# Kernel optimization log

Hardware: AMD Instinct MI355X
Metric: run time of the kernel (lower is better)

The kernel has to match this reference:

```python
import jax, jax.numpy as jnp
import numpy as np

B, T, D_MODEL = 2, 192, 512
N_HEADS, D_HEAD = 8, 64
IGNORE = -1000000.0


def setup_inputs() -> dict:
    key = jax.random.key(0)
    ks = jax.random.split(key, 5)
    s = 0.02
    return {
        "x": jax.random.normal(ks[0], (B, T, D_MODEL), dtype=jnp.float32),
        "Wkkq": jax.random.normal(ks[1], (D_MODEL, 3 * N_HEADS * D_HEAD), dtype=jnp.float32) * s,
        "bkkq": jnp.zeros((3 * N_HEADS * D_HEAD,), jnp.float32),
        "Wv1": jax.random.normal(ks[2], (D_MODEL, N_HEADS * D_HEAD), dtype=jnp.float32) * s,
        "bv1": jnp.zeros((N_HEADS * D_HEAD,), jnp.float32),
        "Wv2": jax.random.normal(ks[3], (D_MODEL, N_HEADS * D_HEAD), dtype=jnp.float32) * s,
        "bv2": jnp.zeros((N_HEADS * D_HEAD,), jnp.float32),
        "Wout": jax.random.normal(ks[4], (N_HEADS * D_HEAD, D_MODEL), dtype=jnp.float32) * s,
        "bout": jnp.zeros((D_MODEL,), jnp.float32),
    }


def reference(x, Wkkq, bkkq, Wv1, bv1, Wv2, bv2, Wout, bout):
    b, ts, _ = x.shape
    kkq = x @ Wkkq + bkkq                          # [b, t, 3*n*h]
    k1, k2, q = jnp.split(kkq, 3, axis=-1)
    rs = lambda a: a.reshape(b, ts, N_HEADS, D_HEAD)  # b p n h
    k1, k2, q = rs(k1), rs(k2), rs(q)

    v1 = (x @ Wv1 + bv1).reshape(b, ts, N_HEADS, D_HEAD)
    v2 = (x @ Wv2 + bv2).reshape(b, ts, N_HEADS, D_HEAD)

    # third-order scores: [b, n, s, t, q]
    score_qk = jnp.einsum('btnh,bqnh->bntq', k2, q)   # [b, n, t, q]
    score_kk = jnp.einsum('bsnh,btnh->bnst', k1, k2)  # [b, n, s, t]
    score = score_qk[:, :, None, :, :] + score_kk[..., None]  # [b,n,s,t,q]

    idx = jnp.arange(ts)
    # causal mask: (t > q) | (s > q)  over axes (s, t, q)
    mask = (idx[:, None, None] > idx[None, None, :]) | (idx[None, :, None] > idx[None, None, :])
    score = jnp.where(mask[None, None], IGNORE, score)

    # b n s t q -> b n q (s t), scale by d_head, softmax over flattened (s,t)
    score = jnp.transpose(score, (0, 1, 4, 2, 3)).reshape(b, N_HEADS, ts, ts * ts)
    attn = jax.nn.softmax(score / D_HEAD, axis=-1)

    # v[b, p, t, n, h] = silu(v1)[b,p,n,h] * v2[b,t,n,h]
    v = jax.nn.silu(v1)[:, :, None] * v2[:, None]     # [b, p, t, n, h]
    v = jnp.transpose(v, (0, 3, 4, 1, 2)).reshape(b, N_HEADS, D_HEAD, ts * ts)

    z = jnp.einsum('bnql,bnhl->bqnh', attn, v)        # [b, q, n, h]
    out = z.reshape(b, ts, N_HEADS * D_HEAD) @ Wout + bout
    return out
```

## Files before the change

kernel.cpp:

```cpp
#include <hip/hip_runtime.h>
#include <hip/hip_bf16.h>


constexpr int Tn = 192;
constexpr int DM = 512;
constexpr int NH = 8;
constexpr int HD = 64;
constexpr int TT = Tn * Tn;
constexpr int NC = 8;
constexpr int CS = 24;

typedef __bf16 bf16_t;
typedef bf16_t bf16x8 __attribute__((ext_vector_type(8)));
typedef bf16_t bf16x4 __attribute__((ext_vector_type(4)));
typedef float  f32x4  __attribute__((ext_vector_type(4)));

struct bf16pair { bf16_t h, l; };
__device__ __forceinline__ bf16pair split_bf16(float v) {
    bf16pair r;
    r.h = (bf16_t)v;
    r.l = (bf16_t)(v - (float)r.h);
    return r;
}

__global__ __launch_bounds__(256) void k_convert(
    const float* __restrict__ x,    const float* __restrict__ Wkkq,
    const float* __restrict__ Wv1,  const float* __restrict__ Wv2,
    const float* __restrict__ Wout,
    bf16_t* __restrict__ xh,    bf16_t* __restrict__ xl,
    bf16_t* __restrict__ wkkqh, bf16_t* __restrict__ wkkql,
    bf16_t* __restrict__ wv1h,  bf16_t* __restrict__ wv1l,
    bf16_t* __restrict__ wv2h,  bf16_t* __restrict__ wv2l,
    bf16_t* __restrict__ wouth, bf16_t* __restrict__ woutl)
{
    const int bid = blockIdx.x;
    const int tid = threadIdx.x;

    if (bid >= 1536) {
        const int idx = (bid - 1536) * 1024 + tid * 4;
        const float4 v = *reinterpret_cast<const float4*>(&x[idx]);
        bf16x4 hv, lv;
        bf16pair p0 = split_bf16(v.x), p1 = split_bf16(v.y);
        bf16pair p2 = split_bf16(v.z), p3 = split_bf16(v.w);
        hv[0] = p0.h; lv[0] = p0.l; hv[1] = p1.h; lv[1] = p1.l;
        hv[2] = p2.h; lv[2] = p2.l; hv[3] = p3.h; lv[3] = p3.l;
        *reinterpret_cast<bf16x4*>(&xh[idx]) = hv;
        *reinterpret_cast<bf16x4*>(&xl[idx]) = lv;
        return;
    }

    const float* src; bf16_t* dh; bf16_t* dl; int N, lb;
    if (bid < 768)       { src = Wkkq; dh = wkkqh; dl = wkkql; N = 1536; lb = bid; }
    else if (bid < 1024) { src = Wv1;  dh = wv1h;  dl = wv1l;  N = 512;  lb = bid - 768; }
    else if (bid < 1280) { src = Wv2;  dh = wv2h;  dl = wv2l;  N = 512;  lb = bid - 1024; }
    else                 { src = Wout; dh = wouth; dl = woutl; N = 512;  lb = bid - 1280; }

    const int ntn = N >> 5;
    const int k0 = (lb / ntn) * 32, n0 = (lb % ntn) * 32;

    __shared__ float T[32][33];
    const int r = tid >> 3, c4 = (tid & 7) * 4;
    const float4 v = *reinterpret_cast<const float4*>(&src[(k0 + r) * N + n0 + c4]);
    T[r][c4] = v.x; T[r][c4 + 1] = v.y; T[r][c4 + 2] = v.z; T[r][c4 + 3] = v.w;
    __syncthreads();

    const int nr = tid >> 3, kc4 = (tid & 7) * 4;
    bf16x4 hv, lv;
#pragma unroll
    for (int i = 0; i < 4; ++i) {
        bf16pair p = split_bf16(T[kc4 + i][nr]);
        hv[i] = p.h; lv[i] = p.l;
    }
    *reinterpret_cast<bf16x4*>(&dh[(n0 + nr) * DM + k0 + kc4]) = hv;
    *reinterpret_cast<bf16x4*>(&dl[(n0 + nr) * DM + k0 + kc4]) = lv;
}

__global__ __launch_bounds__(256) void k_projm(
    const bf16_t* __restrict__ xh,    const bf16_t* __restrict__ xl,
    const bf16_t* __restrict__ wkkqh, const bf16_t* __restrict__ wkkql,
    const bf16_t* __restrict__ wv1h,  const bf16_t* __restrict__ wv1l,
    const bf16_t* __restrict__ wv2h,  const bf16_t* __restrict__ wv2l,
    const float* __restrict__ bkkq, const float* __restrict__ bv1,
    const float* __restrict__ bv2,
    float* __restrict__ k1, float* __restrict__ k2, float* __restrict__ qv,
    float* __restrict__ sv1, float* __restrict__ v2o)
{
    const int bx = blockIdx.x, by = blockIdx.y;
    const int tid = threadIdx.x;
    const int w = tid >> 6, lane = tid & 63;
    const int wm = w & 1, wn = w >> 1;
    const int lr = lane & 15, lk = (lane >> 4) * 8;

    const bf16_t *Bh, *Bl; int nbase;
    if (bx < 24)      { Bh = wkkqh; Bl = wkkql; nbase = bx * 64; }
    else if (bx < 32) { Bh = wv1h;  Bl = wv1l;  nbase = bx * 64 - 1536; }
    else              { Bh = wv2h;  Bl = wv2l;  nbase = bx * 64 - 2048; }

    const int arow  = by * 32 + wm * 16 + lr;
    const int brow0 = nbase + wn * 32 + lr;
    const int brow1 = brow0 + 16;

    f32x4 acc0 = {0.f,0.f,0.f,0.f}, acc1 = {0.f,0.f,0.f,0.f};
    bf16x8 A_ah, A_al, A_b0h, A_b0l, A_b1h, A_b1l;
    bf16x8 B_ah, B_al, B_b0h, B_b0l, B_b1h, B_b1l;

#define PLD(P_, KS) do { const int ko_ = (KS) * 32 + lk;                     \
    P_##ah  = *reinterpret_cast<const bf16x8*>(&xh[arow  * DM + ko_]);       \
    P_##al  = *reinterpret_cast<const bf16x8*>(&xl[arow  * DM + ko_]);       \
    P_##b0h = *reinterpret_cast<const bf16x8*>(&Bh[brow0 * DM + ko_]);       \
    P_##b0l = *reinterpret_cast<const bf16x8*>(&Bl[brow0 * DM + ko_]);       \
    P_##b1h = *reinterpret_cast<const bf16x8*>(&Bh[brow1 * DM + ko_]);       \
    P_##b1l = *reinterpret_cast<const bf16x8*>(&Bl[brow1 * DM + ko_]); } while (0)
#define PMM(P_) do {                                                                      \
    acc0 = __builtin_amdgcn_mfma_f32_16x16x32_bf16(P_##ah, P_##b0h, acc0, 0, 0, 0);       \
    acc0 = __builtin_amdgcn_mfma_f32_16x16x32_bf16(P_##ah, P_##b0l, acc0, 0, 0, 0);       \
    acc0 = __builtin_amdgcn_mfma_f32_16x16x32_bf16(P_##al, P_##b0h, acc0, 0, 0, 0);       \
    acc1 = __builtin_amdgcn_mfma_f32_16x16x32_bf16(P_##ah, P_##b1h, acc1, 0, 0, 0);       \
    acc1 = __builtin_amdgcn_mfma_f32_16x16x32_bf16(P_##ah, P_##b1l, acc1, 0, 0, 0);       \
    acc1 = __builtin_amdgcn_mfma_f32_16x16x32_bf16(P_##al, P_##b1h, acc1, 0, 0, 0); } while (0)

    PLD(A_, 0);
    for (int ks = 0; ks < 14; ks += 2) {
        PLD(B_, ks + 1);
        PMM(A_);
        PLD(A_, ks + 2);
        PMM(B_);
    }
    PLD(B_, 15);
    PMM(A_);
    PMM(B_);
#undef PLD
#undef PMM

#pragma unroll
    for (int ni = 0; ni < 2; ++ni) {
        const f32x4 a4 = ni ? acc1 : acc0;
        const int gcol = bx * 64 + wn * 32 + ni * 16 + lr;
#pragma unroll
        for (int r = 0; r < 4; ++r) {
            const int row = by * 32 + wm * 16 + (lane >> 4) * 4 + r;
            const int b = row / Tn, t = row % Tn;
            const float a = a4[r];
            if (gcol < 1536) {
                const float val = a + bkkq[gcol];
                const int third = gcol >> 9, nh = gcol & 511, n = nh >> 6, hh = nh & 63;
                float* dst = (third == 0) ? k1 : (third == 1) ? k2 : qv;
                dst[((b * NH + n) * Tn + t) * HD + hh] = val;
            } else if (gcol < 2048) {
                const int c = gcol - 1536;
                float val = a + bv1[c];
                val = val / (1.f + __expf(-val));
                sv1[((b * NH + (c >> 6)) * Tn + t) * HD + (c & 63)] = val;
            } else {
                const int c = gcol - 2048;
                v2o[((b * NH + (c >> 6)) * Tn + t) * HD + (c & 63)] = a + bv2[c];
            }
        }
    }
}

__global__ __launch_bounds__(256) void k_scores(
    const float* __restrict__ k1, const float* __restrict__ k2,
    const float* __restrict__ qv,
    float* __restrict__ Ekk, float* __restrict__ Eqk)
{
    const int bn  = blockIdx.z;
    const int mat = blockIdx.y;
    const int st  = blockIdx.x / 6, tt = blockIdx.x % 6;
    const float* A  = ((mat == 0) ? k1 : qv) + bn * Tn * HD;
    const float* Bm = k2 + bn * Tn * HD;
    float* E = ((mat == 0) ? Ekk : Eqk) + bn * TT;

    __shared__ float As[32][65], Bs[32][65];
    const int tid = threadIdx.x;
    for (int i = tid; i < 32 * 64; i += 256) {
        const int r = i >> 6, h = i & 63;
        As[r][h] = A[(st * 32 + r) * HD + h];
        Bs[r][h] = Bm[(tt * 32 + r) * HD + h];
    }
    __syncthreads();

    const int tx = tid & 15, ty = tid >> 4;
    const int r0 = ty * 2, c0 = tx * 2;
    float a00 = 0.f, a01 = 0.f, a10 = 0.f, a11 = 0.f;
#pragma unroll
    for (int h = 0; h < 64; ++h) {
        const float ar0 = As[r0][h], ar1 = As[r0 + 1][h];
        const float bc0 = Bs[c0][h], bc1 = Bs[c0 + 1][h];
        a00 = fmaf(ar0, bc0, a00); a01 = fmaf(ar0, bc1, a01);
        a10 = fmaf(ar1, bc0, a10); a11 = fmaf(ar1, bc1, a11);
    }
    constexpr float sc = 1.f / 64.f;
    const int gr = st * 32 + r0, gc = tt * 32 + c0;
    E[(gr)     * Tn + gc]     = __expf(a00 * sc);
    E[(gr)     * Tn + gc + 1] = __expf(a01 * sc);
    E[(gr + 1) * Tn + gc]     = __expf(a10 * sc);
    E[(gr + 1) * Tn + gc + 1] = __expf(a11 * sc);
}

__global__ __launch_bounds__(256) void k_partial(
    const float* __restrict__ Ekk, const float* __restrict__ sv1,
    float* __restrict__ P)
{
    const int hhalf = blockIdx.x;
    const int c     = blockIdx.y;
    const int bn    = blockIdx.z;
    const int tid   = threadIdx.x;
    const int tg    = tid & 7;
    const int h     = hhalf * 32 + (tid >> 3);
    const int t0    = tg * 24;
    const float* ekk = Ekk + bn * TT;
    const float* s1  = sv1 + bn * Tn * HD;

    float G[24];
#pragma unroll
    for (int j = 0; j < 24; ++j) G[j] = 0.f;

    for (int s = c * CS; s < c * CS + CS; ++s) {
        const float a = s1[s * HD + h];
        const float* ek = ekk + s * Tn + t0;
#pragma unroll
        for (int jj = 0; jj < 6; ++jj) {
            const float4 ev = *reinterpret_cast<const float4*>(&ek[4 * jj]);
            G[4*jj+0] = fmaf(ev.x, a, G[4*jj+0]);
            G[4*jj+1] = fmaf(ev.y, a, G[4*jj+1]);
            G[4*jj+2] = fmaf(ev.z, a, G[4*jj+2]);
            G[4*jj+3] = fmaf(ev.w, a, G[4*jj+3]);
        }
    }
    float* dst = P + ((bn * NC + c) * HD + h) * Tn + t0;
#pragma unroll
    for (int jj = 0; jj < 6; ++jj)
        *reinterpret_cast<float4*>(&dst[4 * jj]) =
            make_float4(G[4*jj], G[4*jj+1], G[4*jj+2], G[4*jj+3]);
}

__global__ __launch_bounds__(256) void k_scangc(
    float* __restrict__ P, const float* __restrict__ Ekk, float* __restrict__ gC)
{
    const int bn = blockIdx.y;
    if (blockIdx.x < 48) {
        const int off = blockIdx.x * 256 + threadIdx.x;
        float* base = P + bn * NC * HD * Tn;
        float run = base[off];
        for (int c = 1; c < NC; ++c) {
            run += base[c * HD * Tn + off];
            base[c * HD * Tn + off] = run;
        }
    } else {
        const int t = threadIdx.x;
        if (t < Tn) {
            const float* ekk = Ekk + bn * TT;
            float sum = 0.f;
            for (int c = 0; c < NC; ++c) {
#pragma unroll
                for (int i = 0; i < CS; ++i)
                    sum += ekk[(c * CS + i) * Tn + t];
                gC[(bn * NC + c) * Tn + t] = sum;
            }
        }
    }
}

__global__ __launch_bounds__(256) void k_attn2(
    const float* __restrict__ Ekk, const float* __restrict__ Eqk,
    const float* __restrict__ sv1, const float* __restrict__ v2,
    const float* __restrict__ P,   const float* __restrict__ gC,
    float* __restrict__ z)
{
    const int hq = blockIdx.x;
    const int qt = blockIdx.y;
    const int bn = blockIdx.z;
    const int b = bn >> 3, n = bn & 7;
    const int tid = threadIdx.x;
    const int tg  = tid & 15;
    const int hh  = tid >> 4;
    const int h   = hq * 16 + hh;
    const int t0  = tg * 12;
    const int q0  = qt * 12;
    const int cb  = q0 / CS;

    const float* ekk = Ekk + bn * TT;
    const float* eqk = Eqk + bn * TT;
    const float* s1  = sv1 + bn * Tn * HD;
    const float* vv  = v2  + bn * Tn * HD;

    float G[12], g[12];
    if (cb > 0) {
        const float* pb = P  + ((bn * NC + (cb - 1)) * HD + h) * Tn + t0;
        const float* gb = gC + (bn * NC + (cb - 1)) * Tn + t0;
#pragma unroll
        for (int jj = 0; jj < 3; ++jj) {
            const float4 pv = *reinterpret_cast<const float4*>(&pb[4 * jj]);
            G[4*jj+0] = pv.x; G[4*jj+1] = pv.y; G[4*jj+2] = pv.z; G[4*jj+3] = pv.w;
            const float4 gv = *reinterpret_cast<const float4*>(&gb[4 * jj]);
            g[4*jj+0] = gv.x; g[4*jj+1] = gv.y; g[4*jj+2] = gv.z; g[4*jj+3] = gv.w;
        }
    } else {
#pragma unroll
        for (int j = 0; j < 12; ++j) { G[j] = 0.f; g[j] = 0.f; }
    }

    float vvr[12];
#pragma unroll
    for (int j = 0; j < 12; ++j) vvr[j] = vv[(t0 + j) * HD + h];

    for (int s = CS * cb; s < q0; ++s) {
        const float a = s1[s * HD + h];
        const float* ek = ekk + s * Tn + t0;
#pragma unroll
        for (int jj = 0; jj < 3; ++jj) {
            const float4 ev = *reinterpret_cast<const float4*>(&ek[4 * jj]);
            G[4*jj+0] = fmaf(ev.x, a, G[4*jj+0]); g[4*jj+0] += ev.x;
            G[4*jj+1] = fmaf(ev.y, a, G[4*jj+1]); g[4*jj+1] += ev.y;
            G[4*jj+2] = fmaf(ev.z, a, G[4*jj+2]); g[4*jj+2] += ev.z;
            G[4*jj+3] = fmaf(ev.w, a, G[4*jj+3]); g[4*jj+3] += ev.w;
        }
    }

    for (int q = q0; q < q0 + 12; ++q) {
        {
            const float a = s1[q * HD + h];
            const float* ek = ekk + q * Tn + t0;
#pragma unroll
            for (int jj = 0; jj < 3; ++jj) {
                const float4 ev = *reinterpret_cast<const float4*>(&ek[4 * jj]);
                G[4*jj+0] = fmaf(ev.x, a, G[4*jj+0]); g[4*jj+0] += ev.x;
                G[4*jj+1] = fmaf(ev.y, a, G[4*jj+1]); g[4*jj+1] += ev.y;
                G[4*jj+2] = fmaf(ev.z, a, G[4*jj+2]); g[4*jj+2] += ev.z;
                G[4*jj+3] = fmaf(ev.w, a, G[4*jj+3]); g[4*jj+3] += ev.w;
            }
        }
        const float* eq = eqk + q * Tn + t0;
        float zp = 0.f, Zp = 0.f;
#pragma unroll
        for (int jj = 0; jj < 3; ++jj) {
            const float4 ev = *reinterpret_cast<const float4*>(&eq[4 * jj]);
            const float e0 = (t0 + 4*jj + 0 <= q) ? ev.x : 0.f;
            const float e1 = (t0 + 4*jj + 1 <= q) ? ev.y : 0.f;
            const float e2 = (t0 + 4*jj + 2 <= q) ? ev.z : 0.f;
            const float e3 = (t0 + 4*jj + 3 <= q) ? ev.w : 0.f;
            zp = fmaf(e0 * vvr[4*jj+0], G[4*jj+0], zp); Zp = fmaf(e0, g[4*jj+0], Zp);
            zp = fmaf(e1 * vvr[4*jj+1], G[4*jj+1], zp); Zp = fmaf(e1, g[4*jj+1], Zp);
            zp = fmaf(e2 * vvr[4*jj+2], G[4*jj+2], zp); Zp = fmaf(e2, g[4*jj+2], Zp);
            zp = fmaf(e3 * vvr[4*jj+3], G[4*jj+3], zp); Zp = fmaf(e3, g[4*jj+3], Zp);
        }
        zp += __shfl_xor(zp, 1); zp += __shfl_xor(zp, 2);
        zp += __shfl_xor(zp, 4); zp += __shfl_xor(zp, 8);
        Zp += __shfl_xor(Zp, 1); Zp += __shfl_xor(Zp, 2);
        Zp += __shfl_xor(Zp, 4); Zp += __shfl_xor(Zp, 8);
        if (tg == 0) z[((b * Tn + q) * NH + n) * HD + h] = zp / Zp;
    }
}

__global__ __launch_bounds__(256) void k_outm(
    const float* __restrict__ z,
    const bf16_t* __restrict__ wouth, const bf16_t* __restrict__ woutl,
    const float* __restrict__ bout, float* __restrict__ out)
{
    const int bx = blockIdx.x, by = blockIdx.y;
    const int tid = threadIdx.x;
    const int w = tid >> 6, lane = tid & 63;
    const int lr = lane & 15, lk = (lane >> 4) * 8;
    const int arow = by * 16 + lr;
    const int brow = bx * 64 + w * 16 + lr;

    f32x4 acc = {0.f,0.f,0.f,0.f};
    bf16x8 A_ah, A_al, A_bh, A_bl;
    bf16x8 B_ah, B_al, B_bh, B_bl;

#define OLD(P_, KS) do { const int ko_ = (KS) * 32 + lk;                       \
    const float4 u0 = *reinterpret_cast<const float4*>(&z[arow * DM + ko_]);   \
    const float4 u1 = *reinterpret_cast<const float4*>(&z[arow * DM + ko_ + 4]); \
    bf16pair q0 = split_bf16(u0.x), q1 = split_bf16(u0.y);                     \
    bf16pair q2 = split_bf16(u0.z), q3 = split_bf16(u0.w);                     \
    bf16pair q4 = split_bf16(u1.x), q5 = split_bf16(u1.y);                     \
    bf16pair q6 = split_bf16(u1.z), q7 = split_bf16(u1.w);                     \
    P_##ah[0] = q0.h; P_##al[0] = q0.l; P_##ah[1] = q1.h; P_##al[1] = q1.l;    \
    P_##ah[2] = q2.h; P_##al[2] = q2.l; P_##ah[3] = q3.h; P_##al[3] = q3.l;    \
    P_##ah[4] = q4.h; P_##al[4] = q4.l; P_##ah[5] = q5.h; P_##al[5] = q5.l;    \
    P_##ah[6] = q6.h; P_##al[6] = q6.l; P_##ah[7] = q7.h; P_##al[7] = q7.l;    \
    P_##bh = *reinterpret_cast<const bf16x8*>(&wouth[brow * DM + ko_]);        \
    P_##bl = *reinterpret_cast<const bf16x8*>(&woutl[brow * DM + ko_]); } while (0)
#define OMM(P_) do {                                                                   \
    acc = __builtin_amdgcn_mfma_f32_16x16x32_bf16(P_##ah, P_##bh, acc, 0, 0, 0);       \
    acc = __builtin_amdgcn_mfma_f32_16x16x32_bf16(P_##ah, P_##bl, acc, 0, 0, 0);       \
    acc = __builtin_amdgcn_mfma_f32_16x16x32_bf16(P_##al, P_##bh, acc, 0, 0, 0); } while (0)

    OLD(A_, 0);
    for (int ks = 0; ks < 14; ks += 2) {
        OLD(B_, ks + 1);
        OMM(A_);
        OLD(A_, ks + 2);
        OMM(B_);
    }
    OLD(B_, 15);
    OMM(A_);
    OMM(B_);
#undef OLD
#undef OMM

    const int col = bx * 64 + w * 16 + lr;
#pragma unroll
    for (int r = 0; r < 4; ++r) {
        const int row = by * 16 + (lane >> 4) * 4 + r;
        out[row * DM + col] = acc[r] + bout[col];
    }
}

extern "C" void kernel_launch(void* const* d_in, const int* in_sizes, int n_in,
                              void* d_out, int out_size, void* d_ws, size_t ws_size,
                              hipStream_t stream) {
    const float* x    = (const float*)d_in[0];
    const float* Wkkq = (const float*)d_in[1];
    const float* bkkq = (const float*)d_in[2];
    const float* Wv1  = (const float*)d_in[3];
    const float* bv1  = (const float*)d_in[4];
    const float* Wv2  = (const float*)d_in[5];
    const float* bv2  = (const float*)d_in[6];
    const float* Wout = (const float*)d_in[7];
    const float* bout = (const float*)d_in[8];
    float* out = (float*)d_out;

    float* ws  = (float*)d_ws;
    float* k1  = ws;
    float* k2  = k1  + 196608;
    float* qv  = k2  + 196608;
    float* sv1 = qv  + 196608;
    float* v2  = sv1 + 196608;
    float* z   = v2  + 196608;
    float* Ekk = z   + 196608;
    float* Eqk = Ekk + 589824;
    float* P   = Eqk + 589824;
    float* gC  = P   + 1572864;
    bf16_t* bws   = (bf16_t*)(gC + 24576);
    bf16_t* xh    = bws;
    bf16_t* xl    = xh    + 196608;
    bf16_t* wkkqh = xl    + 196608;
    bf16_t* wkkql = wkkqh + 786432;
    bf16_t* wv1h  = wkkql + 786432;
    bf16_t* wv1l  = wv1h  + 262144;
    bf16_t* wv2h  = wv1l  + 262144;
    bf16_t* wv2l  = wv2h  + 262144;
    bf16_t* wouth = wv2l  + 262144;
    bf16_t* woutl = wouth + 262144;

    k_convert<<<dim3(1728),      256, 0, stream>>>(x, Wkkq, Wv1, Wv2, Wout,
                                                   xh, xl, wkkqh, wkkql,
                                                   wv1h, wv1l, wv2h, wv2l, wouth, woutl);
    k_projm  <<<dim3(40, 12),    256, 0, stream>>>(xh, xl, wkkqh, wkkql, wv1h, wv1l,
                                                   wv2h, wv2l, bkkq, bv1, bv2,
                                                   k1, k2, qv, sv1, v2);
    k_scores <<<dim3(36, 2, 16), 256, 0, stream>>>(k1, k2, qv, Ekk, Eqk);
    k_partial<<<dim3(2, 8, 16),  256, 0, stream>>>(Ekk, sv1, P);
    k_scangc <<<dim3(49, 16),    256, 0, stream>>>(P, Ekk, gC);
    k_attn2  <<<dim3(4, 16, 16), 256, 0, stream>>>(Ekk, Eqk, sv1, v2, P, gC, z);
    k_outm   <<<dim3(8, 24),     256, 0, stream>>>(z, wouth, woutl, bout, out);
}
```

Before: 98.49 us.

## Fuse partial prefix sums into score kernel and drop scan kernel

```diff
diff --git a/kernel.cpp b/kernel.cpp
--- a/kernel.cpp
+++ b/kernel.cpp
@@ -7,8 +7,8 @@
 constexpr int NH = 8;
 constexpr int HD = 64;
 constexpr int TT = Tn * Tn;
-constexpr int NC = 8;
-constexpr int CS = 24;
+constexpr int NCc = 6;
+constexpr int CSc = 32;
 
 typedef __bf16 bf16_t;
 typedef bf16_t bf16x8 __attribute__((ext_vector_type(8)));
@@ -92,91 +92,83 @@
     const int lr = lane & 15, lk = (lane >> 4) * 8;
 
     const bf16_t *Bh, *Bl; int nbase;
-    if (bx < 24)      { Bh = wkkqh; Bl = wkkql; nbase = bx * 64; }
-    else if (bx < 32) { Bh = wv1h;  Bl = wv1l;  nbase = bx * 64 - 1536; }
-    else              { Bh = wv2h;  Bl = wv2l;  nbase = bx * 64 - 2048; }
-
-    const int arow  = by * 32 + wm * 16 + lr;
-    const int brow0 = nbase + wn * 32 + lr;
-    const int brow1 = brow0 + 16;
-
-    f32x4 acc0 = {0.f,0.f,0.f,0.f}, acc1 = {0.f,0.f,0.f,0.f};
-    bf16x8 A_ah, A_al, A_b0h, A_b0l, A_b1h, A_b1l;
-    bf16x8 B_ah, B_al, B_b0h, B_b0l, B_b1h, B_b1l;
+    if (bx < 48)      { Bh = wkkqh; Bl = wkkql; nbase = bx * 32; }
+    else if (bx < 64) { Bh = wv1h;  Bl = wv1l;  nbase = bx * 32 - 1536; }
+    else              { Bh = wv2h;  Bl = wv2l;  nbase = bx * 32 - 2048; }
+
+    const int arow = by * 32 + wm * 16 + lr;
+    const int brow = nbase + wn * 16 + lr;
+
+    f32x4 acc = {0.f,0.f,0.f,0.f};
+    bf16x8 A_ah, A_al, A_bh, A_bl;
+    bf16x8 B_ah, B_al, B_bh, B_bl;
 
 #define PLD(P_, KS) do { const int ko_ = (KS) * 32 + lk;                     \
-    P_##ah  = *reinterpret_cast<const bf16x8*>(&xh[arow  * DM + ko_]);       \
-    P_##al  = *reinterpret_cast<const bf16x8*>(&xl[arow  * DM + ko_]);       \
-    P_##b0h = *reinterpret_cast<const bf16x8*>(&Bh[brow0 * DM + ko_]);       \
-    P_##b0l = *reinterpret_cast<const bf16x8*>(&Bl[brow0 * DM + ko_]);       \
-    P_##b1h = *reinterpret_cast<const bf16x8*>(&Bh[brow1 * DM + ko_]);       \
-    P_##b1l = *reinterpret_cast<const bf16x8*>(&Bl[brow1 * DM + ko_]); } while (0)
-#define PMM(P_) do {                                                                      \
-    acc0 = __builtin_amdgcn_mfma_f32_16x16x32_bf16(P_##ah, P_##b0h, acc0, 0, 0, 0);       \
-    acc0 = __builtin_amdgcn_mfma_f32_16x16x32_bf16(P_##ah, P_##b0l, acc0, 0, 0, 0);       \
-    acc0 = __builtin_amdgcn_mfma_f32_16x16x32_bf16(P_##al, P_##b0h, acc0, 0, 0, 0);       \
-    acc1 = __builtin_amdgcn_mfma_f32_16x16x32_bf16(P_##ah, P_##b1h, acc1, 0, 0, 0);       \
-    acc1 = __builtin_amdgcn_mfma_f32_16x16x32_bf16(P_##ah, P_##b1l, acc1, 0, 0, 0);       \
-    acc1 = __builtin_amdgcn_mfma_f32_16x16x32_bf16(P_##al, P_##b1h, acc1, 0, 0, 0); } while (0)
-
-    PLD(A_, 0);
-    for (int ks = 0; ks < 14; ks += 2) {
-        PLD(B_, ks + 1);
-        PMM(A_);
-        PLD(A_, ks + 2);
-        PMM(B_);
-    }
-    PLD(B_, 15);
-    PMM(A_);
-    PMM(B_);
+    P_##ah = *reinterpret_cast<const bf16x8*>(&xh[arow * DM + ko_]);         \
+    P_##al = *reinterpret_cast<const bf16x8*>(&xl[arow * DM + ko_]);         \
+    P_##bh = *reinterpret_cast<const bf16x8*>(&Bh[brow * DM + ko_]);         \
+    P_##bl = *reinterpret_cast<const bf16x8*>(&Bl[brow * DM + ko_]); } while (0)
+#define PMM(P_) do {                                                                    \
+    acc = __builtin_amdgcn_mfma_f32_16x16x32_bf16(P_##ah, P_##bh, acc, 0, 0, 0);        \
+    acc = __builtin_amdgcn_mfma_f32_16x16x32_bf16(P_##ah, P_##bl, acc, 0, 0, 0);        \
+    acc = __builtin_amdgcn_mfma_f32_16x16x32_bf16(P_##al, P_##bh, acc, 0, 0, 0); } while (0)
+#define PSTEP(P_, KN) do { PMM(P_); if ((KN) < 16) PLD(P_, KN); } while (0)
+
+    PLD(A_, 0); PLD(B_, 1);
+    PSTEP(A_, 2);  PSTEP(B_, 3);  PSTEP(A_, 4);  PSTEP(B_, 5);
+    PSTEP(A_, 6);  PSTEP(B_, 7);  PSTEP(A_, 8);  PSTEP(B_, 9);
+    PSTEP(A_, 10); PSTEP(B_, 11); PSTEP(A_, 12); PSTEP(B_, 13);
+    PSTEP(A_, 14); PSTEP(B_, 15); PSTEP(A_, 16); PSTEP(B_, 17);
 #undef PLD
 #undef PMM
-
-#pragma unroll
-    for (int ni = 0; ni < 2; ++ni) {
-        const f32x4 a4 = ni ? acc1 : acc0;
-        const int gcol = bx * 64 + wn * 32 + ni * 16 + lr;
-#pragma unroll
-        for (int r = 0; r < 4; ++r) {
-            const int row = by * 32 + wm * 16 + (lane >> 4) * 4 + r;
-            const int b = row / Tn, t = row % Tn;
-            const float a = a4[r];
-            if (gcol < 1536) {
-                const float val = a + bkkq[gcol];
-                const int third = gcol >> 9, nh = gcol & 511, n = nh >> 6, hh = nh & 63;
-                float* dst = (third == 0) ? k1 : (third == 1) ? k2 : qv;
-                dst[((b * NH + n) * Tn + t) * HD + hh] = val;
-            } else if (gcol < 2048) {
-                const int c = gcol - 1536;
-                float val = a + bv1[c];
-                val = val / (1.f + __expf(-val));
-                sv1[((b * NH + (c >> 6)) * Tn + t) * HD + (c & 63)] = val;
-            } else {
-                const int c = gcol - 2048;
-                v2o[((b * NH + (c >> 6)) * Tn + t) * HD + (c & 63)] = a + bv2[c];
-            }
-        }
-    }
-}
-
-__global__ __launch_bounds__(256) void k_scores(
+#undef PSTEP
+
+    const int gcol = bx * 32 + wn * 16 + lr;
+#pragma unroll
+    for (int r = 0; r < 4; ++r) {
+        const int row = by * 32 + wm * 16 + (lane >> 4) * 4 + r;
+        const int b = row / Tn, t = row % Tn;
+        const float a = acc[r];
+        if (gcol < 1536) {
+            const float val = a + bkkq[gcol];
+            const int third = gcol >> 9, nh = gcol & 511, n = nh >> 6, hh = nh & 63;
+            float* dst = (third == 0) ? k1 : (third == 1) ? k2 : qv;
+            dst[((b * NH + n) * Tn + t) * HD + hh] = val;
+        } else if (gcol < 2048) {
+            const int c = gcol - 1536;
+            float val = a + bv1[c];
+            val = val / (1.f + __expf(-val));
+            sv1[((b * NH + (c >> 6)) * Tn + t) * HD + (c & 63)] = val;
+        } else {
+            const int c = gcol - 2048;
+            v2o[((b * NH + (c >> 6)) * Tn + t) * HD + (c & 63)] = a + bv2[c];
+        }
+    }
+}
+
+__global__ __launch_bounds__(256) void k_scoresP(
     const float* __restrict__ k1, const float* __restrict__ k2,
-    const float* __restrict__ qv,
-    float* __restrict__ Ekk, float* __restrict__ Eqk)
+    const float* __restrict__ qv, const float* __restrict__ sv1,
+    float* __restrict__ Ekk, float* __restrict__ Eqk,
+    float* __restrict__ P, float* __restrict__ gP)
 {
-    const int bn  = blockIdx.z;
-    const int mat = blockIdx.y;
-    const int st  = blockIdx.x / 6, tt = blockIdx.x % 6;
+    const int bn = blockIdx.y;
+    int bx = blockIdx.x;
+    const int mat = (bx >= 36) ? 1 : 0;
+    if (mat) bx -= 36;
+    const int st = bx / 6, tt = bx % 6;
     const float* A  = ((mat == 0) ? k1 : qv) + bn * Tn * HD;
     const float* Bm = k2 + bn * Tn * HD;
     float* E = ((mat == 0) ? Ekk : Eqk) + bn * TT;
 
-    __shared__ float As[32][65], Bs[32][65];
+    __shared__ float As[32][65], Bs[32][65], Vs[32][65];
+    __shared__ float Es[32][33];
     const int tid = threadIdx.x;
     for (int i = tid; i < 32 * 64; i += 256) {
         const int r = i >> 6, h = i & 63;
         As[r][h] = A[(st * 32 + r) * HD + h];
         Bs[r][h] = Bm[(tt * 32 + r) * HD + h];
+        if (mat == 0) Vs[r][h] = sv1[bn * Tn * HD + (st * 32 + r) * HD + h];
     }
     __syncthreads();
 
@@ -191,73 +183,36 @@
         a10 = fmaf(ar1, bc0, a10); a11 = fmaf(ar1, bc1, a11);
     }
     constexpr float sc = 1.f / 64.f;
+    const float e00 = __expf(a00 * sc), e01 = __expf(a01 * sc);
+    const float e10 = __expf(a10 * sc), e11 = __expf(a11 * sc);
     const int gr = st * 32 + r0, gc = tt * 32 + c0;
-    E[(gr)     * Tn + gc]     = __expf(a00 * sc);
-    E[(gr)     * Tn + gc + 1] = __expf(a01 * sc);
-    E[(gr + 1) * Tn + gc]     = __expf(a10 * sc);
-    E[(gr + 1) * Tn + gc + 1] = __expf(a11 * sc);
-}
-
-__global__ __launch_bounds__(256) void k_partial(
-    const float* __restrict__ Ekk, const float* __restrict__ sv1,
-    float* __restrict__ P)
-{
-    const int hhalf = blockIdx.x;
-    const int c     = blockIdx.y;
-    const int bn    = blockIdx.z;
-    const int tid   = threadIdx.x;
-    const int tg    = tid & 7;
-    const int h     = hhalf * 32 + (tid >> 3);
-    const int t0    = tg * 24;
-    const float* ekk = Ekk + bn * TT;
-    const float* s1  = sv1 + bn * Tn * HD;
-
-    float G[24];
-#pragma unroll
-    for (int j = 0; j < 24; ++j) G[j] = 0.f;
-
-    for (int s = c * CS; s < c * CS + CS; ++s) {
-        const float a = s1[s * HD + h];
-        const float* ek = ekk + s * Tn + t0;
-#pragma unroll
-        for (int jj = 0; jj < 6; ++jj) {
-            const float4 ev = *reinterpret_cast<const float4*>(&ek[4 * jj]);
-            G[4*jj+0] = fmaf(ev.x, a, G[4*jj+0]);
-            G[4*jj+1] = fmaf(ev.y, a, G[4*jj+1]);
-            G[4*jj+2] = fmaf(ev.z, a, G[4*jj+2]);
-            G[4*jj+3] = fmaf(ev.w, a, G[4*jj+3]);
-        }
-    }
-    float* dst = P + ((bn * NC + c) * HD + h) * Tn + t0;
-#pragma unroll
-    for (int jj = 0; jj < 6; ++jj)
-        *reinterpret_cast<float4*>(&dst[4 * jj]) =
-            make_float4(G[4*jj], G[4*jj+1], G[4*jj+2], G[4*jj+3]);
-}
-
-__global__ __launch_bounds__(256) void k_scangc(
-    float* __restrict__ P, const float* __restrict__ Ekk, float* __restrict__ gC)
-{
-    const int bn = blockIdx.y;
-    if (blockIdx.x < 48) {
-        const int off = blockIdx.x * 256 + threadIdx.x;
-        float* base = P + bn * NC * HD * Tn;
-        float run = base[off];
-        for (int c = 1; c < NC; ++c) {
-            run += base[c * HD * Tn + off];
-            base[c * HD * Tn + off] = run;
-        }
-    } else {
-        const int t = threadIdx.x;
-        if (t < Tn) {
-            const float* ekk = Ekk + bn * TT;
-            float sum = 0.f;
-            for (int c = 0; c < NC; ++c) {
-#pragma unroll
-                for (int i = 0; i < CS; ++i)
-                    sum += ekk[(c * CS + i) * Tn + t];
-                gC[(bn * NC + c) * Tn + t] = sum;
-            }
+    E[(gr)     * Tn + gc]     = e00;
+    E[(gr)     * Tn + gc + 1] = e01;
+    E[(gr + 1) * Tn + gc]     = e10;
+    E[(gr + 1) * Tn + gc + 1] = e11;
+
+    if (mat == 0) {
+        Es[r0][c0] = e00; Es[r0][c0 + 1] = e01;
+        Es[r0 + 1][c0] = e10; Es[r0 + 1][c0 + 1] = e11;
+        __syncthreads();
+
+        const int h   = tid >> 2;
+        const int tp0 = (tid & 3) * 8;
+        float p[8] = {0.f,0.f,0.f,0.f,0.f,0.f,0.f,0.f};
+        for (int s = 0; s < 32; ++s) {
+            const float a = Vs[s][h];
+#pragma unroll
+            for (int j = 0; j < 8; ++j) p[j] = fmaf(Es[s][tp0 + j], a, p[j]);
+        }
+        float* pd = P + ((bn * NCc + st) * HD + h) * Tn + tt * 32 + tp0;
+        *reinterpret_cast<float4*>(&pd[0]) = make_float4(p[0], p[1], p[2], p[3]);
+        *reinterpret_cast<float4*>(&pd[4]) = make_float4(p[4], p[5], p[6], p[7]);
+
+        if (tid < 32) {
+            float s = 0.f;
+#pragma unroll
+            for (int ss = 0; ss < 32; ++ss) s += Es[ss][tid];
+            gP[(bn * NCc + st) * Tn + tt * 32 + tid] = s;
         }
     }
 }
@@ -265,7 +220,7 @@
 __global__ __launch_bounds__(256) void k_attn2(
     const float* __restrict__ Ekk, const float* __restrict__ Eqk,
     const float* __restrict__ sv1, const float* __restrict__ v2,
-    const float* __restrict__ P,   const float* __restrict__ gC,
+    const float* __restrict__ P,   const float* __restrict__ gP,
     float* __restrict__ z)
 {
     const int hq = blockIdx.x;
@@ -278,7 +233,7 @@
     const int h   = hq * 16 + hh;
     const int t0  = tg * 12;
     const int q0  = qt * 12;
-    const int cb  = q0 / CS;
+    const int cb  = q0 >> 5;
 
     const float* ekk = Ekk + bn * TT;
     const float* eqk = Eqk + bn * TT;
@@ -286,26 +241,26 @@
     const float* vv  = v2  + bn * Tn * HD;
 
     float G[12], g[12];
-    if (cb > 0) {
-        const float* pb = P  + ((bn * NC + (cb - 1)) * HD + h) * Tn + t0;
-        const float* gb = gC + (bn * NC + (cb - 1)) * Tn + t0;
+#pragma unroll
+    for (int j = 0; j < 12; ++j) { G[j] = 0.f; g[j] = 0.f; }
+
+    for (int c = 0; c < cb; ++c) {
+        const float* pb = P  + ((bn * NCc + c) * HD + h) * Tn + t0;
+        const float* gb = gP + (bn * NCc + c) * Tn + t0;
 #pragma unroll
         for (int jj = 0; jj < 3; ++jj) {
             const float4 pv = *reinterpret_cast<const float4*>(&pb[4 * jj]);
-            G[4*jj+0] = pv.x; G[4*jj+1] = pv.y; G[4*jj+2] = pv.z; G[4*jj+3] = pv.w;
+            G[4*jj+0] += pv.x; G[4*jj+1] += pv.y; G[4*jj+2] += pv.z; G[4*jj+3] += pv.w;
             const float4 gv = *reinterpret_cast<const float4*>(&gb[4 * jj]);
-            g[4*jj+0] = gv.x; g[4*jj+1] = gv.y; g[4*jj+2] = gv.z; g[4*jj+3] = gv.w;
-        }
-    } else {
-#pragma unroll
-        for (int j = 0; j < 12; ++j) { G[j] = 0.f; g[j] = 0.f; }
+            g[4*jj+0] += gv.x; g[4*jj+1] += gv.y; g[4*jj+2] += gv.z; g[4*jj+3] += gv.w;
+        }
     }
 
     float vvr[12];
 #pragma unroll
     for (int j = 0; j < 12; ++j) vvr[j] = vv[(t0 + j) * HD + h];
 
-    for (int s = CS * cb; s < q0; ++s) {
+    for (int s = CSc * cb; s < q0; ++s) {
         const float a = s1[s * HD + h];
         const float* ek = ekk + s * Tn + t0;
 #pragma unroll
@@ -369,36 +324,33 @@
     bf16x8 A_ah, A_al, A_bh, A_bl;
     bf16x8 B_ah, B_al, B_bh, B_bl;
 
-#define OLD(P_, KS) do { const int ko_ = (KS) * 32 + lk;                       \
-    const float4 u0 = *reinterpret_cast<const float4*>(&z[arow * DM + ko_]);   \
+#define OLD(P_, KS) do { const int ko_ = (KS) * 32 + lk;                         \
+    const float4 u0 = *reinterpret_cast<const float4*>(&z[arow * DM + ko_]);     \
     const float4 u1 = *reinterpret_cast<const float4*>(&z[arow * DM + ko_ + 4]); \
-    bf16pair q0 = split_bf16(u0.x), q1 = split_bf16(u0.y);                     \
-    bf16pair q2 = split_bf16(u0.z), q3 = split_bf16(u0.w);                     \
-    bf16pair q4 = split_bf16(u1.x), q5 = split_bf16(u1.y);                     \
-    bf16pair q6 = split_bf16(u1.z), q7 = split_bf16(u1.w);                     \
-    P_##ah[0] = q0.h; P_##al[0] = q0.l; P_##ah[1] = q1.h; P_##al[1] = q1.l;    \
-    P_##ah[2] = q2.h; P_##al[2] = q2.l; P_##ah[3] = q3.h; P_##al[3] = q3.l;    \
-    P_##ah[4] = q4.h; P_##al[4] = q4.l; P_##ah[5] = q5.h; P_##al[5] = q5.l;    \
-    P_##ah[6] = q6.h; P_##al[6] = q6.l; P_##ah[7] = q7.h; P_##al[7] = q7.l;    \
-    P_##bh = *reinterpret_cast<const bf16x8*>(&wouth[brow * DM + ko_]);        \
+    bf16pair q0 = split_bf16(u0.x), q1 = split_bf16(u0.y);                       \
+    bf16pair q2 = split_bf16(u0.z), q3 = split_bf16(u0.w);                       \
+    bf16pair q4 = split_bf16(u1.x), q5 = split_bf16(u1.y);                       \
+    bf16pair q6 = split_bf16(u1.z), q7 = split_bf16(u1.w);                       \
+    P_##ah[0] = q0.h; P_##al[0] = q0.l; P_##ah[1] = q1.h; P_##al[1] = q1.l;      \
+    P_##ah[2] = q2.h; P_##al[2] = q2.l; P_##ah[3] = q3.h; P_##al[3] = q3.l;      \
+    P_##ah[4] = q4.h; P_##al[4] = q4.l; P_##ah[5] = q5.h; P_##al[5] = q5.l;      \
+    P_##ah[6] = q6.h; P_##al[6] = q6.l; P_##ah[7] = q7.h; P_##al[7] = q7.l;      \
+    P_##bh = *reinterpret_cast<const bf16x8*>(&wouth[brow * DM + ko_]);          \
     P_##bl = *reinterpret_cast<const bf16x8*>(&woutl[brow * DM + ko_]); } while (0)
 #define OMM(P_) do {                                                                   \
     acc = __builtin_amdgcn_mfma_f32_16x16x32_bf16(P_##ah, P_##bh, acc, 0, 0, 0);       \
     acc = __builtin_amdgcn_mfma_f32_16x16x32_bf16(P_##ah, P_##bl, acc, 0, 0, 0);       \
     acc = __builtin_amdgcn_mfma_f32_16x16x32_bf16(P_##al, P_##bh, acc, 0, 0, 0); } while (0)
-
-    OLD(A_, 0);
-    for (int ks = 0; ks < 14; ks += 2) {
-        OLD(B_, ks + 1);
-        OMM(A_);
-        OLD(A_, ks + 2);
-        OMM(B_);
-    }
-    OLD(B_, 15);
-    OMM(A_);
-    OMM(B_);
+#define OSTEP(P_, KN) do { OMM(P_); if ((KN) < 16) OLD(P_, KN); } while (0)
+
+    OLD(A_, 0); OLD(B_, 1);
+    OSTEP(A_, 2);  OSTEP(B_, 3);  OSTEP(A_, 4);  OSTEP(B_, 5);
+    OSTEP(A_, 6);  OSTEP(B_, 7);  OSTEP(A_, 8);  OSTEP(B_, 9);
+    OSTEP(A_, 10); OSTEP(B_, 11); OSTEP(A_, 12); OSTEP(B_, 13);
+    OSTEP(A_, 14); OSTEP(B_, 15); OSTEP(A_, 16); OSTEP(B_, 17);
 #undef OLD
 #undef OMM
+#undef OSTEP
 
     const int col = bx * 64 + w * 16 + lr;
 #pragma unroll
@@ -432,8 +384,8 @@
     float* Ekk = z   + 196608;
     float* Eqk = Ekk + 589824;
     float* P   = Eqk + 589824;
-    float* gC  = P   + 1572864;
-    bf16_t* bws   = (bf16_t*)(gC + 24576);
+    float* gP  = P   + 1179648;
+    bf16_t* bws   = (bf16_t*)(gP + 18432);
     bf16_t* xh    = bws;
     bf16_t* xl    = xh    + 196608;
     bf16_t* wkkqh = xl    + 196608;
@@ -448,12 +400,10 @@
     k_convert<<<dim3(1728),      256, 0, stream>>>(x, Wkkq, Wv1, Wv2, Wout,
                                                    xh, xl, wkkqh, wkkql,
                                                    wv1h, wv1l, wv2h, wv2l, wouth, woutl);
-    k_projm  <<<dim3(40, 12),    256, 0, stream>>>(xh, xl, wkkqh, wkkql, wv1h, wv1l,
+    k_projm  <<<dim3(80, 12),    256, 0, stream>>>(xh, xl, wkkqh, wkkql, wv1h, wv1l,
                                                    wv2h, wv2l, bkkq, bv1, bv2,
                                                    k1, k2, qv, sv1, v2);
-    k_scores <<<dim3(36, 2, 16), 256, 0, stream>>>(k1, k2, qv, Ekk, Eqk);
-    k_partial<<<dim3(2, 8, 16),  256, 0, stream>>>(Ekk, sv1, P);
-    k_scangc <<<dim3(49, 16),    256, 0, stream>>>(P, Ekk, gC);
-    k_attn2  <<<dim3(4, 16, 16), 256, 0, stream>>>(Ekk, Eqk, sv1, v2, P, gC, z);
+    k_scoresP<<<dim3(72, 16),    256, 0, stream>>>(k1, k2, qv, sv1, Ekk, Eqk, P, gP);
+    k_attn2  <<<dim3(4, 16, 16), 256, 0, stream>>>(Ekk, Eqk, sv1, v2, P, gP, z);
     k_outm   <<<dim3(8, 24),     256, 0, stream>>>(z, wouth, woutl, bout, out);
 }
```

Measured after the change: 99.82 us. Within noise of the previous version (+1.3%).
